# Performance work log

Measured on AMD Instinct MI355X. Metric: run time of the kernel, lower is better.

The kernel has to match this reference:

```python
import jax, jax.numpy as jnp
import numpy as np

B = 512      # molecules
F = 256      # FPSize
PH = 512     # ProjectHeadSize
H = 256      # TransformerHiddenSize
FFN = 1024   # TransformerFFNSize
NH = 8       # TransformerNumHeads
L = 2        # TransformerEncoderLayers
MAXP = 24    # max singlebond_num
EPS_BN = 1e-6
EPS_LN = 1e-5

def _make_ragged():
    sbn = (np.arange(B) % MAXP) + 1            # deterministic ragged sizes, all >= 1
    pair_mol = np.repeat(np.arange(B), sbn)
    pair_pos = np.concatenate([np.arange(n) for n in sbn])
    return sbn, pair_mol, pair_pos

def setup_inputs():
    sbn, pm, pp = _make_ragged()
    P = int(sbn.sum())  # 6336 fragment pairs
    keys = iter(jax.random.split(jax.random.key(0), 64))
    def lin(fi, fo):
        return (jax.random.normal(next(keys), (fi, fo), jnp.float32) / np.sqrt(fi),
                jnp.zeros((fo,), jnp.float32))
    d = {}
    d['mol_emb'] = jax.random.normal(next(keys), (B, F), jnp.float32)
    d['frag_emb_raw'] = jax.random.normal(next(keys), (2 * P, F), jnp.float32)
    for p in ('mol', 'frag', 'view'):
        d[p + '_W1'], d[p + '_b1'] = lin(F, PH)
        d[p + '_g'] = jnp.ones((PH,), jnp.float32)
        d[p + '_be'] = jnp.zeros((PH,), jnp.float32)
        d[p + '_W2'], d[p + '_b2'] = lin(PH, PH // 2)
    d['enc_in_W'], d['enc_in_b'] = lin(F, H)
    d['enc_out_W'], d['enc_out_b'] = lin(H, F)
    def stk(fi, fo):
        return (jax.random.normal(next(keys), (L, fi, fo), jnp.float32) / np.sqrt(fi),
                jnp.zeros((L, fo), jnp.float32))
    d['Wq'], d['bq'] = stk(H, H)
    d['Wk'], d['bk'] = stk(H, H)
    d['Wv'], d['bv'] = stk(H, H)
    d['Wo'], d['bo'] = stk(H, H)
    d['Wf1'], d['bf1'] = stk(H, FFN)
    d['Wf2'], d['bf2'] = stk(FFN, H)
    d['ln1_g'] = jnp.ones((L, H), jnp.float32); d['ln1_b'] = jnp.zeros((L, H), jnp.float32)
    d['ln2_g'] = jnp.ones((L, H), jnp.float32); d['ln2_b'] = jnp.zeros((L, H), jnp.float32)
    d['singlebond_num'] = jnp.asarray(sbn, jnp.int32)
    d['pair_mol_idx'] = jnp.asarray(pm, jnp.int32)
    d['pair_pos_idx'] = jnp.asarray(pp, jnp.int32)
    return d

def _ln(x, g, b):
    mu = x.mean(-1, keepdims=True)
    v = ((x - mu) ** 2).mean(-1, keepdims=True)
    return (x - mu) * jax.lax.rsqrt(v + EPS_LN) * g + b

def _proj_head(x, W1, b1, g, be, W2, b2):
    # Linear -> BatchNorm1d (train-mode batch stats, eps=1e-6) -> ReLU -> Linear (dropout=identity in eval)
    h = x @ W1 + b1
    mu = h.mean(0)
    v = h.var(0)
    h = jax.nn.relu((h - mu) * jax.lax.rsqrt(v + EPS_BN) * g + be)
    return h @ W2 + b2

def _l2norm(x):
    return x / jnp.maximum(jnp.linalg.norm(x, axis=1, keepdims=True), 1e-12)

def _attn(x, Wq, bq, Wk, bk, Wv, bv, Wo, bo):
    b, s, _ = x.shape
    dh = H // NH
    q = (x @ Wq + bq).reshape(b, s, NH, dh)
    k = (x @ Wk + bk).reshape(b, s, NH, dh)
    v = (x @ Wv + bv).reshape(b, s, NH, dh)
    a = jax.nn.softmax(jnp.einsum('bqhd,bkhd->bhqk', q, k) / np.sqrt(dh), axis=-1)
    return jnp.einsum('bhqk,bkhd->bqhd', a, v).reshape(b, s, H) @ Wo + bo

def reference(mol_emb, frag_emb_raw,
              mol_W1, mol_b1, mol_g, mol_be, mol_W2, mol_b2,
              frag_W1, frag_b1, frag_g, frag_be, frag_W2, frag_b2,
              view_W1, view_b1, view_g, view_be, view_W2, view_b2,
              enc_in_W, enc_in_b, enc_out_W, enc_out_b,
              ln1_g, ln1_b, Wq, bq, Wk, bk, Wv, bv, Wo, bo,
              ln2_g, ln2_b, Wf1, bf1, Wf2, bf2,
              singlebond_num, pair_mol_idx, pair_pos_idx):
    mol_proj = _l2norm(_proj_head(mol_emb, mol_W1, mol_b1, mol_g, mol_be, mol_W2, mol_b2))
    # sum the two complementary fragment embeddings per single bond: view(P,2,F).sum(1)
    P = frag_emb_raw.shape[0] // 2
    pairs = frag_emb_raw.reshape(P, 2, F).sum(axis=1)  # [P, F]
    frag_proj = _l2norm(_proj_head(pairs, frag_W1, frag_b1, frag_g, frag_be, frag_W2, frag_b2))
    sim = frag_proj @ frag_proj.T  # [P, P] pairwise dot-sim
    # ragged pack into [B, MAXP, F] (zero padding, no attention mask, as in original)
    batched = jnp.zeros((B, MAXP, F), pairs.dtype).at[pair_mol_idx, pair_pos_idx].set(pairs)
    h = batched @ enc_in_W + enc_in_b
    for l in range(L):  # pre-LN encoder layers (Graphormer-style EncoderLayer)
        h = h + _attn(_ln(h, ln1_g[l], ln1_b[l]), Wq[l], bq[l], Wk[l], bk[l], Wv[l], bv[l], Wo[l], bo[l])
        y = _ln(h, ln2_g[l], ln2_b[l])
        h = h + (jax.nn.gelu(y @ Wf1[l] + bf1[l]) @ Wf2[l] + bf2[l])
    enc = h @ enc_out_W + enc_out_b  # [B, MAXP, F]
    counts = jnp.maximum(singlebond_num, 1)
    mask = (jnp.arange(MAXP)[None, :] < counts[:, None]).astype(enc.dtype)
    readout = (enc * mask[:, :, None]).sum(axis=1) / counts[:, None].astype(enc.dtype)
    view_proj = _l2norm(_proj_head(readout, view_W1, view_b1, view_g, view_be, view_W2, view_b2))
    return (mol_proj, view_proj, sim)
```

## Files before the change

kernel.cpp:

```cpp
#include <hip/hip_runtime.h>
#include <hip/hip_bf16.h>

#define B_    512
#define F_    256
#define PH_   512
#define PH2_  256
#define H_    256
#define FFN_  1024
#define NH_   8
#define DH_   32
#define L_    2
#define MAXP_ 24
#define T_    (B_*MAXP_)
#define P_    6336
#define NFLT  5878016

typedef __hip_bfloat16 bf16;
typedef __attribute__((ext_vector_type(8))) short short8;
typedef __attribute__((ext_vector_type(4))) float floatx4;
typedef __attribute__((ext_vector_type(4))) ushort ushortx4;

__device__ float  g_arena[5*1024*1024];
__device__ float  g_small[1<<20];
__device__ float  g_par[6*1024*1024];
__device__ ushort g_parb[6*1024*1024];
__device__ ushort g_bf[41*1024*1024];
__device__ int    g_flag[4];

__device__ __forceinline__ float  u2f(ushort u){ return __uint_as_float(((unsigned)u)<<16); }
__device__ __forceinline__ ushort f2u(float f){ return __bfloat16_as_ushort(__float2bfloat16(f)); }

__device__ __forceinline__ void gll16(const ushort* g, ushort* l){
  __builtin_amdgcn_global_load_lds((const __attribute__((address_space(1))) void*)g,
                                   (__attribute__((address_space(3))) void*)l, 16, 0, 0);
}

__device__ const int d_coff[41] = {
  0,131072,3375104,3506176,3506688,3507200,3507712,3638784,3639040,3770112,
  3770624,3771136,3771648,3902720,3902976,4034048,4034560,4035072,4035584,4166656,
  4166912,4232448,4232704,4298240,4298496,4429568,4430080,4561152,4561664,4692736,
  4693248,4824320,4824832,5349120,5351168,5875456,5875968,5876480,5876992,5877504,
  5878016};

__device__ const int t_src[20] = {3375104,3507712,3639040,3771648,3902976,4035584,4166912,4232704,
  4298496,4430080,4561664,4364032,4495616,4627200,4693248,4758784,4824832,5086976,5351168,5613312};
__device__ const int t_dst[20] = {0,131072,262144,393216,524288,655360,786432,851968,
  917504,983040,1048576,1114112,1179648,1245184,1310720,1376256,1441792,1703936,1966080,2228224};
__device__ const int t_K[20] = {256,512,256,512,256,512,256,256,256,256,256,256,256,256,256,256,256,256,1024,1024};
__device__ const int t_N[20] = {512,256,512,256,512,256,256,256,256,256,256,256,256,256,256,256,1024,1024,256,256};
__device__ const int t_tp[21] = {0,32,64,96,128,160,192,208,224,240,256,272,288,304,320,336,352,416,480,544,608};

struct Ptrs { const void* p[40]; };

__global__ __launch_bounds__(256) void FraSICL_42322607735332_kernel(const unsigned* __restrict__ molg,
                                                                     float* __restrict__ batched0,
                                                                     float* __restrict__ stats){
  int i = blockIdx.x*256 + threadIdx.x;
  if (i == 0) g_flag[0] = (molg[0] == 0x3F803F80u) ? 1 : 0;
  if (i < 3*1024) stats[i] = 0.f;
  if (i < T_*H_/2) batched0[i] = 0.f;
}

__global__ __launch_bounds__(256) void k_cast_all(Ptrs ps, float* __restrict__ of, ushort* __restrict__ ob){
  int i = (blockIdx.x*256 + threadIdx.x) * 4;
  if (i >= NFLT) return;
  int lo = 0, hi = 40;
  while (lo + 1 < hi){ int mid = (lo+hi)>>1; if (i >= d_coff[mid]) lo = mid; else hi = mid; }
  int local = i - d_coff[lo];
  float4 v;
  if (g_flag[0]){
    ushortx4 u = *(const ushortx4*)((const ushort*)ps.p[lo] + local);
    v.x = u2f(u[0]); v.y = u2f(u[1]); v.z = u2f(u[2]); v.w = u2f(u[3]);
  } else {
    v = *(const float4*)((const float*)ps.p[lo] + local);
  }
  *(float4*)(of + i) = v;
  ushortx4 o; o[0]=f2u(v.x); o[1]=f2u(v.y); o[2]=f2u(v.z); o[3]=f2u(v.w);
  *(ushortx4*)(ob + i) = o;
}

__global__ __launch_bounds__(256) void k_wtT(const ushort* __restrict__ src, ushort* __restrict__ dst,
                                             const float* __restrict__ par, float* __restrict__ bqkv){
  __shared__ ushort tile[64*65];
  int b = blockIdx.x;
  if (b >= 608){
    int i = (b - 608)*256 + threadIdx.x;
    if (i < 2*768){
      int l = i / 768, n = i % 768;
      const float* s = (n < 256) ? par + 4429568 + l*256 + n
                     : (n < 512) ? par + 4561152 + l*256 + (n-256)
                                 : par + 4692736 + l*256 + (n-512);
      bqkv[i] = *s;
    }
    return;
  }
  int lo = 0, hi = 20;
  while (lo + 1 < hi){ int mid = (lo+hi)>>1; if (b >= t_tp[mid]) lo = mid; else hi = mid; }
  int lt = b - t_tp[lo];
  int K = t_K[lo], N = t_N[lo];
  int tn = N >> 6;
  int k0 = (lt / tn) << 6, n0 = (lt % tn) << 6;
  const ushort* sseg = src + t_src[lo];
  ushort* dseg = dst + t_dst[lo];
  int t = threadIdx.x;
  #pragma unroll
  for (int j = 0; j < 16; j++){
    int idx = t + j*256;
    int r = idx >> 6, c = idx & 63;
    tile[r*65 + c] = sseg[(size_t)(k0 + r)*N + n0 + c];
  }
  __syncthreads();
  #pragma unroll
  for (int j = 0; j < 16; j++){
    int idx = t + j*256;
    int on = idx >> 6, ok = idx & 63;
    dseg[(size_t)(n0 + on)*K + k0 + ok] = tile[ok*65 + on];
  }
}

__global__ void k_pairs_scatter(const float* __restrict__ frag, const int* __restrict__ pm,
                                const int* __restrict__ pp, ushort* __restrict__ pairs,
                                ushort* __restrict__ batched){
  int p = blockIdx.x, f = threadIdx.x;
  float v = frag[(size_t)(2*p)*F_ + f] + frag[(size_t)(2*p+1)*F_ + f];
  ushort u = f2u(v);
  pairs[(size_t)p*F_ + f] = u;
  batched[(size_t)(pm[p]*MAXP_ + pp[p])*H_ + f] = u;
}

__global__ __launch_bounds__(256) void k_mfma(const ushort* __restrict__ A, const ushort* __restrict__ Bm,
                                              const float* __restrict__ bias, void* __restrict__ Cv,
                                              size_t coff, int M, int N, int K, int act, int mode, int sym,
                                              float* __restrict__ stats)
{
  __shared__ ushort smem[17408];
  ushort* As_ = smem;
  ushort* Bs_ = smem + 4096;
  int tid = threadIdx.x;
  int wave = tid >> 6, lane = tid & 63;
  int wrow = (wave >> 1) * 64, wcol = (wave & 1) * 64;
  int quad = lane >> 4, l16 = lane & 15;
  int m0 = blockIdx.y * 128, n0 = blockIdx.x * 128;
  if (sym && m0 > n0) return;

  int srow = (wave << 5) + (lane >> 2);
  int scol = (lane & 3) << 3;
  int lbase = (wave << 5) * 32;

  floatx4 acc[4][4];
  #pragma unroll
  for (int i = 0; i < 4; i++)
    #pragma unroll
    for (int j = 0; j < 4; j++) acc[i][j] = (floatx4){0.f,0.f,0.f,0.f};

  for (int k0 = 0; k0 < K; k0 += 32){
    {
      int r0 = m0 + srow;      if (r0 > M-1) r0 = M-1;
      int r1 = m0 + srow + 16; if (r1 > M-1) r1 = M-1;
      gll16(A + (size_t)r0*K + k0 + scol, As_ + lbase);
      gll16(A + (size_t)r1*K + k0 + scol, As_ + lbase + 512);
      int q0 = n0 + srow;      if (q0 > N-1) q0 = N-1;
      int q1 = n0 + srow + 16; if (q1 > N-1) q1 = N-1;
      gll16(Bm + (size_t)q0*K + k0 + scol, Bs_ + lbase);
      gll16(Bm + (size_t)q1*K + k0 + scol, Bs_ + lbase + 512);
    }
    __syncthreads();
    short8 af[4], bfr[4];
    #pragma unroll
    for (int mi = 0; mi < 4; mi++) af[mi]  = *(short8*)&As_[(wrow + mi*16 + l16)*32 + quad*8];
    #pragma unroll
    for (int nj = 0; nj < 4; nj++) bfr[nj] = *(short8*)&Bs_[(wcol + nj*16 + l16)*32 + quad*8];
    #pragma unroll
    for (int mi = 0; mi < 4; mi++)
      #pragma unroll
      for (int nj = 0; nj < 4; nj++)
        acc[mi][nj] = __builtin_amdgcn_mfma_f32_16x16x32_bf16(af[mi], bfr[nj], acc[mi][nj], 0, 0, 0);
    __syncthreads();
  }

  int isbf = g_flag[0];
  bool bfpath = (mode == 2) || (mode == 3 && isbf);
  if (!bfpath){
    #pragma unroll
    for (int nj = 0; nj < 4; nj++){
      int col = n0 + wcol + nj*16 + l16;
      float ss = 0.f, ss2 = 0.f;
      #pragma unroll
      for (int mi = 0; mi < 4; mi++){
        #pragma unroll
        for (int r = 0; r < 4; r++){
          int row = m0 + wrow + mi*16 + quad*4 + r;
          if (row < M && col < N){
            float v = acc[mi][nj][r];
            if (bias) v += bias[col];
            if (act == 1) v = fmaxf(v, 0.f);
            else if (act == 2){
              float t = v + 0.044715f*v*v*v;
              v = 0.5f*v*(1.f + tanhf(0.7978845608028654f*t));
            }
            size_t idx = coff + (size_t)row*N + col;
            if (mode == 1) ((float*)Cv)[idx] += v; else ((float*)Cv)[idx] = v;
            if (sym && m0 != n0) ((float*)Cv)[coff + (size_t)col*N + row] = v;
            ss += v; ss2 += v*v;
          }
        }
      }
      if (stats && col < N){
        atomicAdd(&stats[col], ss);
        atomicAdd(&stats[N + col], ss2);
      }
    }
  } else {
    __syncthreads();
    ushort* Cs = smem;
    #pragma unroll
    for (int mi = 0; mi < 4; mi++)
      #pragma unroll
      for (int nj = 0; nj < 4; nj++){
        int lc = wcol + nj*16 + l16;
        int col = n0 + lc;
        #pragma unroll
        for (int r = 0; r < 4; r++){
          int lr = wrow + mi*16 + quad*4 + r;
          float v = acc[mi][nj][r];
          if (bias && col < N) v += bias[col];
          if (act == 1) v = fmaxf(v, 0.f);
          else if (act == 2){
            float t = v + 0.044715f*v*v*v;
            v = 0.5f*v*(1.f + tanhf(0.7978845608028654f*t));
          }
          Cs[lr*136 + lc] = f2u(v);
        }
      }
    __syncthreads();
    ushort* outp = (ushort*)Cv + coff;
    #pragma unroll
    for (int p = 0; p < 8; p++){
      int lr  = p*16 + (tid >> 4);
      int lcs = (tid & 15) * 8;
      int grow = m0 + lr, gcol = n0 + lcs;
      if (grow < M && gcol < N){
        if (gcol + 8 <= N)
          *(uint4*)(outp + (size_t)grow*N + gcol) = *(uint4*)&Cs[lr*136 + lcs];
        else
          for (int u = 0; u < N - gcol; u++) outp[(size_t)grow*N + gcol + u] = Cs[lr*136 + lcs + u];
      }
    }
    if (sym && m0 != n0){
      #pragma unroll
      for (int p = 0; p < 8; p++){
        int lr  = p*16 + (tid >> 4);
        int lcs = (tid & 15) * 8;
        int grow = n0 + lr, gcol = m0 + lcs;
        if (grow < N && gcol < M){
          ushort t8[8];
          #pragma unroll
          for (int u = 0; u < 8; u++) t8[u] = Cs[(lcs + u)*136 + lr];
          if (gcol + 8 <= M)
            *(uint4*)(outp + (size_t)grow*N + gcol) = *(uint4*)t8;
          else
            for (int u = 0; u < M - gcol; u++) outp[(size_t)grow*N + gcol + u] = t8[u];
        }
      }
    }
  }
}

#define SXf 260
#define SQe 776
#define SAe 264

template<int EPI>
__device__ __forceinline__ void enc_gemm(
    float* __restrict__ xr, ushort* __restrict__ qkvs, ushort* __restrict__ a2,
    const ushort* __restrict__ A_lds, const ushort* __restrict__ Bg, int ldb,
    const float* __restrict__ bias, int qc0, int wave, int lane)
{
  int l16 = lane & 15, quad = lane >> 4;
  floatx4 acc[2][4];
  #pragma unroll
  for (int i = 0; i < 2; i++)
    #pragma unroll
    for (int j = 0; j < 4; j++) acc[i][j] = (floatx4){0.f,0.f,0.f,0.f};

  const ushort* bp[4];
  #pragma unroll
  for (int nj = 0; nj < 4; nj++)
    bp[nj] = Bg + (size_t)(wave*64 + nj*16 + l16)*ldb + quad*8;

  #pragma unroll
  for (int kk = 0; kk < 8; kk++){
    short8 af[2], bfr[4];
    #pragma unroll
    for (int nj = 0; nj < 4; nj++) bfr[nj] = *(const short8*)(bp[nj] + kk*32);
    #pragma unroll
    for (int mi = 0; mi < 2; mi++) af[mi] = *(short8*)&A_lds[(mi*16 + l16)*SAe + kk*32 + quad*8];
    #pragma unroll
    for (int mi = 0; mi < 2; mi++)
      #pragma unroll
      for (int nj = 0; nj < 4; nj++)
        acc[mi][nj] = __builtin_amdgcn_mfma_f32_16x16x32_bf16(af[mi], bfr[nj], acc[mi][nj], 0, 0, 0);
  }

  #pragma unroll
  for (int mi = 0; mi < 2; mi++)
    #pragma unroll
    for (int nj = 0; nj < 4; nj++){
      int col = wave*64 + nj*16 + l16;
      #pragma unroll
      for (int r = 0; r < 4; r++){
        int row = mi*16 + quad*4 + r;
        float v = acc[mi][nj][r];
        if (EPI == 0){ if (row < 24) xr[row*SXf + col] = v + bias[col]; }
        else if (EPI == 1){ if (row < 24) qkvs[row*SQe + qc0 + col] = f2u(v + bias[col]); }
        else if (EPI == 2){ if (row < 24) xr[row*SXf + col] += bias ? (v + bias[col]) : v; }
        else {
          float t = v + bias[col];
          float u = t + 0.044715f*t*t*t;
          t = 0.5f*t*(1.f + tanhf(0.7978845608028654f*u));
          a2[row*SAe + col] = f2u(t);
        }
      }
    }
  __syncthreads();
}

__device__ __forceinline__ void enc_ln(const float* __restrict__ xr, ushort* __restrict__ abf,
    const float* __restrict__ g, const float* __restrict__ bv, int wave, int lane)
{
  for (int rr = wave; rr < 24; rr += 4){
    float4 v = *(const float4*)&xr[rr*SXf + lane*4];
    float s1 = v.x+v.y+v.z+v.w;
    float s2 = v.x*v.x+v.y*v.y+v.z*v.z+v.w*v.w;
    #pragma unroll
    for (int o = 32; o > 0; o >>= 1){ s1 += __shfl_down(s1, o, 64); s2 += __shfl_down(s2, o, 64); }
    s1 = __shfl(s1, 0, 64); s2 = __shfl(s2, 0, 64);
    float mu = s1 * (1.f/256.f);
    float rI = rsqrtf(s2 * (1.f/256.f) - mu*mu + 1e-5f);
    float4 gg = *(const float4*)(g + lane*4);
    float4 bb = *(const float4*)(bv + lane*4);
    ushortx4 o4;
    o4[0] = f2u((v.x-mu)*rI*gg.x + bb.x);
    o4[1] = f2u((v.y-mu)*rI*gg.y + bb.y);
    o4[2] = f2u((v.z-mu)*rI*gg.z + bb.z);
    o4[3] = f2u((v.w-mu)*rI*gg.w + bb.w);
    *(ushortx4*)&abf[rr*SAe + lane*4] = o4;
  }
  __syncthreads();
}

__device__ __forceinline__ void enc_attn(const ushort* __restrict__ qkvs, ushort* __restrict__ abf,
                                         int wave, int lane)
{
  int role = (lane < 24) ? 0 : ((lane >= 32 && lane < 56) ? 1 : -1);
  if (role >= 0){
    int r = lane - role*32;
    int h = wave*2 + role;
    int qb = h*32;
    float q[32];
    #pragma unroll
    for (int d8 = 0; d8 < 4; d8++){
      short8 qv = *(const short8*)&qkvs[r*SQe + qb + d8*8];
      #pragma unroll
      for (int u = 0; u < 8; u++) q[d8*8+u] = u2f((ushort)qv[u]);
    }
    float s[24]; float mx = -1e30f;
    #pragma unroll
    for (int j = 0; j < 24; j++){
      float a = 0.f;
      #pragma unroll
      for (int d8 = 0; d8 < 4; d8++){
        short8 kv = *(const short8*)&qkvs[j*SQe + 256 + qb + d8*8];
        #pragma unroll
        for (int u = 0; u < 8; u++) a += q[d8*8+u]*u2f((ushort)kv[u]);
      }
      s[j] = a * 0.17677669529663687f;
      mx = fmaxf(mx, s[j]);
    }
    float sum = 0.f;
    #pragma unroll
    for (int j = 0; j < 24; j++){ s[j] = __expf(s[j]-mx); sum += s[j]; }
    float inv = 1.f/sum;
    float o[32];
    #pragma unroll
    for (int d = 0; d < 32; d++) o[d] = 0.f;
    #pragma unroll
    for (int j = 0; j < 24; j++){
      #pragma unroll
      for (int d8 = 0; d8 < 4; d8++){
        short8 vv = *(const short8*)&qkvs[j*SQe + 512 + qb + d8*8];
        #pragma unroll
        for (int u = 0; u < 8; u++) o[d8*8+u] += s[j]*u2f((ushort)vv[u]);
      }
    }
    #pragma unroll
    for (int d8 = 0; d8 < 4; d8++){
      short8 ov;
      #pragma unroll
      for (int u = 0; u < 8; u++) ov[u] = (short)f2u(o[d8*8+u]*inv);
      *(short8*)&abf[r*SAe + qb + d8*8] = ov;
    }
  }
  __syncthreads();
}

__global__ __launch_bounds__(256, 2) void k_encoder(
    const ushort* __restrict__ batched, const int* __restrict__ sbn,
    const ushort* __restrict__ encinT, const float* __restrict__ enc_in_b,
    const ushort* __restrict__ qkvT, const float* __restrict__ bqkv,
    const ushort* __restrict__ WoT, const float* __restrict__ bo,
    const ushort* __restrict__ Wf1T, const float* __restrict__ bf1,
    const ushort* __restrict__ Wf2T, const float* __restrict__ bf2,
    const float* __restrict__ ln1g, const float* __restrict__ ln1b,
    const float* __restrict__ ln2g, const float* __restrict__ ln2b,
    const ushort* __restrict__ encoutT, const float* __restrict__ enc_out_b,
    ushort* __restrict__ ro)
{
  __shared__ float  xr[24*SXf];
  __shared__ ushort qkvs[24*SQe];
  __shared__ ushort abf[32*SAe];

  int b = blockIdx.x;
  int tid = threadIdx.x;
  int wave = tid >> 6, lane = tid & 63;
  ushort* a2 = qkvs;

  {
    short8 z = {0,0,0,0,0,0,0,0};
    for (int i = tid; i < 32*SAe/8; i += 256) *(short8*)&abf[i*8] = z;
  }
  {
    const ushort* Ag = batched + (size_t)b*24*256;
    #pragma unroll
    for (int i = 0; i < 3; i++){
      int e = (i*256 + tid)*8;
      short8 v = *(const short8*)(Ag + e);
      int row = e >> 8, col = e & 255;
      *(short8*)&abf[row*SAe + col] = v;
    }
  }
  __syncthreads();

  enc_gemm<0>(xr, qkvs, a2, abf, encinT, 256, enc_in_b, 0, wave, lane);

  #pragma unroll 1
  for (int l = 0; l < 2; l++){
    enc_ln(xr, abf, ln1g + l*256, ln1b + l*256, wave, lane);
    #pragma unroll 1
    for (int c = 0; c < 3; c++)
      enc_gemm<1>(xr, qkvs, a2, abf, qkvT + l*196608 + c*65536, 256,
                  bqkv + l*768 + c*256, c*256, wave, lane);
    enc_attn(qkvs, abf, wave, lane);
    enc_gemm<2>(xr, qkvs, a2, abf, WoT + l*65536, 256, bo + l*256, 0, wave, lane);
    enc_ln(xr, abf, ln2g + l*256, ln2b + l*256, wave, lane);
    #pragma unroll 1
    for (int c = 0; c < 4; c++){
      enc_gemm<3>(xr, qkvs, a2, abf, Wf1T + l*262144 + c*65536, 256,
                  bf1 + l*1024 + c*256, 0, wave, lane);
      enc_gemm<2>(xr, qkvs, a2, a2, Wf2T + l*262144 + c*256, 1024,
                  (c == 0) ? (bf2 + l*256) : (const float*)nullptr, 0, wave, lane);
    }
  }

  int cnum = sbn[b]; if (cnum < 1) cnum = 1;
  float* rd = (float*)abf;
  if (tid < 256){
    float s = 0.f;
    for (int p = 0; p < cnum; p++) s += xr[p*SXf + tid];
    rd[tid] = s / (float)cnum;
  }
  __syncthreads();
  {
    float a = enc_out_b[tid];
    const ushort* wr = encoutT + (size_t)tid*256;
    #pragma unroll
    for (int s8 = 0; s8 < 32; s8++){
      short8 wv = *(const short8*)(wr + s8*8);
      #pragma unroll
      for (int u = 0; u < 8; u++) a += rd[s8*8+u]*u2f((ushort)wv[u]);
    }
    ro[(size_t)b*256 + tid] = f2u(a);
  }
}

__global__ void k_bn_apply_bf(const float* __restrict__ h, const float* __restrict__ stats,
                              const float* __restrict__ g, const float* __restrict__ be,
                              ushort* __restrict__ ob, int N, float invM){
  int col = blockIdx.y*256 + threadIdx.x;
  float mu  = stats[col] * invM;
  float var = stats[N + col] * invM - mu*mu;
  float inv = rsqrtf(var + 1e-6f);
  size_t i = (size_t)blockIdx.x*N + col;
  float v = (h[i] - mu) * inv * g[col] + be[col];
  ob[i] = f2u(fmaxf(v, 0.f));
}

__global__ __launch_bounds__(256) void k_l2n_out(const float* __restrict__ x, void* __restrict__ outv,
                                                 size_t elem_off){
  int row = blockIdx.x, t = threadIdx.x;
  float v = x[(size_t)row*256 + t];
  float s = v*v;
  #pragma unroll
  for (int o = 32; o > 0; o >>= 1) s += __shfl_down(s, o, 64);
  __shared__ float red[4];
  int wave = t >> 6, lane = t & 63;
  if (lane == 0) red[wave] = s;
  __syncthreads();
  if (t == 0) red[0] = red[0]+red[1]+red[2]+red[3];
  __syncthreads();
  float sc = 1.f / fmaxf(sqrtf(red[0]), 1e-12f);
  float o = v * sc;
  size_t idx = elem_off + (size_t)row*256 + t;
  if (g_flag[0]) ((bf16*)outv)[idx] = __float2bfloat16(o);
  else           ((float*)outv)[idx] = o;
}

__global__ __launch_bounds__(256) void k_l2n_bfout(const float* __restrict__ x, ushort* __restrict__ ob){
  int wave = threadIdx.x >> 6, lane = threadIdx.x & 63;
  size_t row = (size_t)blockIdx.x*4 + wave;
  const float4 v = *(const float4*)(x + row*256 + lane*4);
  float s = v.x*v.x+v.y*v.y+v.z*v.z+v.w*v.w;
  #pragma unroll
  for (int o = 32; o > 0; o >>= 1) s += __shfl_down(s, o, 64);
  s = __shfl(s, 0, 64);
  float sc = 1.f / fmaxf(sqrtf(s), 1e-12f);
  ushortx4 o4;
  o4[0] = f2u(v.x*sc); o4[1] = f2u(v.y*sc); o4[2] = f2u(v.z*sc); o4[3] = f2u(v.w*sc);
  *(ushortx4*)(ob + row*256 + lane*4) = o4;
}


extern "C" void kernel_launch(void* const* d_in, const int* in_sizes, int n_in,
                              void* d_out, int out_size, void* d_ws, size_t ws_size,
                              hipStream_t stream) {
  (void)in_sizes; (void)n_in; (void)d_ws; (void)ws_size; (void)out_size;

  void *p_arena=nullptr,*p_small=nullptr,*p_par=nullptr,*p_parb=nullptr,*p_bf=nullptr;
  hipGetSymbolAddress(&p_arena, HIP_SYMBOL(g_arena));
  hipGetSymbolAddress(&p_small, HIP_SYMBOL(g_small));
  hipGetSymbolAddress(&p_par,   HIP_SYMBOL(g_par));
  hipGetSymbolAddress(&p_parb,  HIP_SYMBOL(g_parb));
  hipGetSymbolAddress(&p_bf,    HIP_SYMBOL(g_bf));
  float*  arena = (float*)p_arena;
  float*  small = (float*)p_small;
  float*  par   = (float*)p_par;
  ushort* parb  = (ushort*)p_parb;
  ushort* bfb   = (ushort*)p_bf;

  const float *mol_b1=par+3506176, *mol_g=par+3506688, *mol_be=par+3507200, *mol_b2=par+3638784;
  const float *frag_b1=par+3770112, *frag_g=par+3770624, *frag_be=par+3771136, *frag_b2=par+3902720;
  const float *view_b1=par+4034048, *view_g=par+4034560, *view_be=par+4035072, *view_b2=par+4166656;
  const float *enc_in_b=par+4232448, *enc_out_b=par+4298240;
  const float *bo=par+4824320, *bf1=par+5349120, *bf2=par+5875456;
  const float *ln1_g=par+5875968, *ln1_b=par+5876480, *ln2_g=par+5876992, *ln2_b=par+5877504;
  const ushort *molemb_b = parb + 0;
  const float  *frag_f   = par  + 131072;
  const int* sbn = (const int*)d_in[40];
  const int* pm  = (const int*)d_in[41];
  const int* pp  = (const int*)d_in[42];

  ushort* WT = bfb + 38469632;
  const ushort *molW1T=WT+0, *molW2T=WT+131072, *fragW1T=WT+262144, *fragW2T=WT+393216;
  const ushort *viewW1T=WT+524288, *viewW2T=WT+655360, *encinT=WT+786432, *encoutT=WT+851968;
  const ushort *qkvT=WT+917504, *WoT=WT+1310720, *Wf1T=WT+1441792, *Wf2T=WT+1966080;

  const size_t TH = (size_t)T_*H_;
  ushort* pairs_bf    = bfb;
  ushort* fragh1_bf   = bfb + 1622016;
  ushort* fragproj_bf = bfb + 4866048;
  ushort* batched_bf  = bfb + 6488064;
  ushort* ro_bf       = bfb + 38076416;
  ushort* h1b_bf      = bfb + 38207488;
  float* fragh1_f = arena;
  float* fragproj = arena + 3244032;
  float* tmp  = small;
  float* h1b  = small + 131072;
  float* stats= small + 393216;
  float* statsMol  = stats;
  float* statsFrag = stats + 1024;
  float* statsView = stats + 2048;
  float* bqkvf = small + 427008;

  const size_t OFF_MOL  = 0;
  const size_t OFF_VIEW = (size_t)B_*PH2_;
  const size_t OFF_SIM  = 2*(size_t)B_*PH2_;

  FraSICL_42322607735332_kernel<<<(int)(TH/2+255)/256, 256, 0, stream>>>(
      (const unsigned*)d_in[4], (float*)batched_bf, stats);
  Ptrs ps;
  for (int i = 0; i < 40; i++) ps.p[i] = d_in[i];
  k_cast_all<<<(NFLT/4+255)/256, 256, 0, stream>>>(ps, par, parb);
  k_wtT<<<614, 256, 0, stream>>>(parb, bfb + 38469632, par, bqkvf);

  k_mfma<<<dim3(PH_/128, B_/128), 256, 0, stream>>>(molemb_b, molW1T, mol_b1, h1b, 0, B_, PH_, F_, 0, 0, 0, statsMol);
  k_bn_apply_bf<<<dim3(B_, PH_/256), 256, 0, stream>>>(h1b, statsMol, mol_g, mol_be, h1b_bf, PH_, 1.f/B_);
  k_mfma<<<dim3(PH2_/128, B_/128), 256, 0, stream>>>(h1b_bf, molW2T, mol_b2, tmp, 0, B_, PH2_, PH_, 0, 0, 0, nullptr);
  k_l2n_out<<<B_, 256, 0, stream>>>(tmp, d_out, OFF_MOL);

  k_pairs_scatter<<<P_, 256, 0, stream>>>(frag_f, pm, pp, pairs_bf, batched_bf);
  k_mfma<<<dim3(PH_/128, (P_+127)/128), 256, 0, stream>>>(pairs_bf, fragW1T, frag_b1, fragh1_f, 0, P_, PH_, F_, 0, 0, 0, statsFrag);
  k_bn_apply_bf<<<dim3(P_, PH_/256), 256, 0, stream>>>(fragh1_f, statsFrag, frag_g, frag_be, fragh1_bf, PH_, 1.f/P_);
  k_mfma<<<dim3(PH2_/128, (P_+127)/128), 256, 0, stream>>>(fragh1_bf, fragW2T, frag_b2, fragproj, 0, P_, PH2_, PH_, 0, 0, 0, nullptr);
  k_l2n_bfout<<<P_/4, 256, 0, stream>>>(fragproj, fragproj_bf);
  k_mfma<<<dim3((P_+127)/128, (P_+127)/128), 256, 0, stream>>>(fragproj_bf, fragproj_bf, nullptr, d_out, OFF_SIM, P_, P_, PH2_, 0, 3, 1, nullptr);

  k_encoder<<<B_, 256, 0, stream>>>(batched_bf, sbn,
      encinT, enc_in_b, qkvT, bqkvf, WoT, bo, Wf1T, bf1, Wf2T, bf2,
      ln1_g, ln1_b, ln2_g, ln2_b, encoutT, enc_out_b, ro_bf);

  k_mfma<<<dim3(PH_/128, B_/128), 256, 0, stream>>>(ro_bf, viewW1T, view_b1, h1b, 0, B_, PH_, F_, 0, 0, 0, statsView);
  k_bn_apply_bf<<<dim3(B_, PH_/256), 256, 0, stream>>>(h1b, statsView, view_g, view_be, h1b_bf, PH_, 1.f/B_);
  k_mfma<<<dim3(PH2_/128, B_/128), 256, 0, stream>>>(h1b_bf, viewW2T, view_b2, tmp, 0, B_, PH2_, PH_, 0, 0, 0, nullptr);
  k_l2n_out<<<B_, 256, 0, stream>>>(tmp, d_out, OFF_VIEW);
}
```

Baseline: 821.7 us.

## Pack encoder weights into MFMA fragment order and use cheaper GELU tanh

Adds a k_wpack kernel that rearranges the encoder weights (enc_in, QKV, Wo, FFN1, FFN2) into 16x32 tiles laid out in MFMA fragment order, so each lane in enc_gemm loads its B fragment from one contiguous 16-byte chunk instead of strided rows. The GELU epilogue computes tanh through __expf, and the enc_out projection now reads the original row-major weights with a strided per-column access. The unused act==2 path is removed from k_mfma. This costs one extra small packing launch per call, and the GELU result differs slightly numerically.

```diff
diff --git a/kernel.cpp b/kernel.cpp
--- a/kernel.cpp
+++ b/kernel.cpp
@@ -50,6 +50,14 @@
 __device__ const int t_N[20] = {512,256,512,256,512,256,256,256,256,256,256,256,256,256,256,256,1024,1024,256,256};
 __device__ const int t_tp[21] = {0,32,64,96,128,160,192,208,224,240,256,272,288,304,320,336,352,416,480,544,608};
 
+__device__ const int w_src[13] = {4166912,4298496,4430080,4561664,4364032,4495616,4627200,
+  4693248,4758784,4824832,5086976,5351168,5613312};
+__device__ const int w_dst[13] = {0,65536,131072,196608,262144,327680,393216,
+  458752,524288,589824,851968,1114112,1376256};
+__device__ const int w_K[13] = {256,256,256,256,256,256,256,256,256,256,256,1024,1024};
+__device__ const int w_N[13] = {256,256,256,256,256,256,256,256,256,1024,1024,256,256};
+__device__ const int w_tp[14] = {0,16,32,48,64,80,96,112,128,144,208,272,336,400};
+
 struct Ptrs { const void* p[40]; };
 
 __global__ __launch_bounds__(256) void FraSICL_42322607735332_kernel(const unsigned* __restrict__ molg,
@@ -115,6 +123,39 @@
     int idx = t + j*256;
     int on = idx >> 6, ok = idx & 63;
     dseg[(size_t)(n0 + on)*K + k0 + ok] = tile[ok*65 + on];
+  }
+}
+
+__global__ __launch_bounds__(256) void k_wpack(const ushort* __restrict__ src, ushort* __restrict__ dst){
+  __shared__ ushort tile[64*65];
+  int b = blockIdx.x;
+  int lo = 0, hi = 13;
+  while (lo + 1 < hi){ int mid = (lo+hi)>>1; if (b >= w_tp[mid]) lo = mid; else hi = mid; }
+  int lt = b - w_tp[lo];
+  int K = w_K[lo], N = w_N[lo];
+  int nn = N >> 6;
+  int k0 = (lt / nn) << 6, n0 = (lt % nn) << 6;
+  const ushort* s = src + w_src[lo];
+  int t = threadIdx.x;
+  #pragma unroll
+  for (int j = 0; j < 16; j++){
+    int idx = t + j*256;
+    int r = idx >> 6, c = idx & 63;
+    tile[r*65 + c] = s[(size_t)(k0 + r)*N + n0 + c];
+  }
+  __syncthreads();
+  int KT = K >> 5;
+  ushort* d = dst + w_dst[lo];
+  #pragma unroll
+  for (int i = 0; i < 8; i++){
+    int ntl = i >> 1, ktl = i & 1;
+    size_t base = ((size_t)((n0 >> 4) + ntl) * KT + (k0 >> 5) + ktl) * 512;
+    #pragma unroll
+    for (int j = 0; j < 2; j++){
+      int off = t + j*256;
+      int quad = off >> 7, l16 = (off >> 3) & 15, e = off & 7;
+      d[base + off] = tile[(ktl*32 + quad*8 + e)*65 + ntl*16 + l16];
+    }
   }
 }
 
@@ -194,10 +235,6 @@
             float v = acc[mi][nj][r];
             if (bias) v += bias[col];
             if (act == 1) v = fmaxf(v, 0.f);
-            else if (act == 2){
-              float t = v + 0.044715f*v*v*v;
-              v = 0.5f*v*(1.f + tanhf(0.7978845608028654f*t));
-            }
             size_t idx = coff + (size_t)row*N + col;
             if (mode == 1) ((float*)Cv)[idx] += v; else ((float*)Cv)[idx] = v;
             if (sym && m0 != n0) ((float*)Cv)[coff + (size_t)col*N + row] = v;
@@ -225,10 +262,6 @@
           float v = acc[mi][nj][r];
           if (bias && col < N) v += bias[col];
           if (act == 1) v = fmaxf(v, 0.f);
-          else if (act == 2){
-            float t = v + 0.044715f*v*v*v;
-            v = 0.5f*v*(1.f + tanhf(0.7978845608028654f*t));
-          }
           Cs[lr*136 + lc] = f2u(v);
         }
       }
@@ -273,7 +306,7 @@
 template<int EPI>
 __device__ __forceinline__ void enc_gemm(
     float* __restrict__ xr, ushort* __restrict__ qkvs, ushort* __restrict__ a2,
-    const ushort* __restrict__ A_lds, const ushort* __restrict__ Bg, int ldb,
+    const ushort* __restrict__ A_lds, const ushort* __restrict__ pk, int KT, int nt0, int kt0,
     const float* __restrict__ bias, int qc0, int wave, int lane)
 {
   int l16 = lane & 15, quad = lane >> 4;
@@ -286,13 +319,13 @@
   const ushort* bp[4];
   #pragma unroll
   for (int nj = 0; nj < 4; nj++)
-    bp[nj] = Bg + (size_t)(wave*64 + nj*16 + l16)*ldb + quad*8;
+    bp[nj] = pk + ((size_t)(nt0 + wave*4 + nj)*KT + kt0)*512 + lane*8;
 
   #pragma unroll
   for (int kk = 0; kk < 8; kk++){
     short8 af[2], bfr[4];
     #pragma unroll
-    for (int nj = 0; nj < 4; nj++) bfr[nj] = *(const short8*)(bp[nj] + kk*32);
+    for (int nj = 0; nj < 4; nj++) bfr[nj] = *(const short8*)(bp[nj] + kk*512);
     #pragma unroll
     for (int mi = 0; mi < 2; mi++) af[mi] = *(short8*)&A_lds[(mi*16 + l16)*SAe + kk*32 + quad*8];
     #pragma unroll
@@ -315,10 +348,11 @@
         else if (EPI == 1){ if (row < 24) qkvs[row*SQe + qc0 + col] = f2u(v + bias[col]); }
         else if (EPI == 2){ if (row < 24) xr[row*SXf + col] += bias ? (v + bias[col]) : v; }
         else {
-          float t = v + bias[col];
-          float u = t + 0.044715f*t*t*t;
-          t = 0.5f*t*(1.f + tanhf(0.7978845608028654f*u));
-          a2[row*SAe + col] = f2u(t);
+          float t0 = v + bias[col];
+          float u = 0.7978845608028654f*(t0 + 0.044715f*t0*t0*t0);
+          float e = __expf(2.f*u);
+          float th = 1.f - 2.f/(e + 1.f);
+          a2[row*SAe + col] = f2u(0.5f*t0*(1.f + th));
         }
       }
     }
@@ -406,14 +440,14 @@
 
 __global__ __launch_bounds__(256, 2) void k_encoder(
     const ushort* __restrict__ batched, const int* __restrict__ sbn,
-    const ushort* __restrict__ encinT, const float* __restrict__ enc_in_b,
-    const ushort* __restrict__ qkvT, const float* __restrict__ bqkv,
-    const ushort* __restrict__ WoT, const float* __restrict__ bo,
-    const ushort* __restrict__ Wf1T, const float* __restrict__ bf1,
-    const ushort* __restrict__ Wf2T, const float* __restrict__ bf2,
+    const ushort* __restrict__ encinP, const float* __restrict__ enc_in_b,
+    const ushort* __restrict__ qkvP, const float* __restrict__ bqkv,
+    const ushort* __restrict__ WoP, const float* __restrict__ bo,
+    const ushort* __restrict__ Wf1P, const float* __restrict__ bf1,
+    const ushort* __restrict__ Wf2P, const float* __restrict__ bf2,
     const float* __restrict__ ln1g, const float* __restrict__ ln1b,
     const float* __restrict__ ln2g, const float* __restrict__ ln2b,
-    const ushort* __restrict__ encoutT, const float* __restrict__ enc_out_b,
+    const ushort* __restrict__ encoutO, const float* __restrict__ enc_out_b,
     ushort* __restrict__ ro)
 {
   __shared__ float  xr[24*SXf];
@@ -441,23 +475,23 @@
   }
   __syncthreads();
 
-  enc_gemm<0>(xr, qkvs, a2, abf, encinT, 256, enc_in_b, 0, wave, lane);
+  enc_gemm<0>(xr, qkvs, a2, abf, encinP, 8, 0, 0, enc_in_b, 0, wave, lane);
 
   #pragma unroll 1
   for (int l = 0; l < 2; l++){
     enc_ln(xr, abf, ln1g + l*256, ln1b + l*256, wave, lane);
     #pragma unroll 1
     for (int c = 0; c < 3; c++)
-      enc_gemm<1>(xr, qkvs, a2, abf, qkvT + l*196608 + c*65536, 256,
+      enc_gemm<1>(xr, qkvs, a2, abf, qkvP + l*196608 + c*65536, 8, 0, 0,
                   bqkv + l*768 + c*256, c*256, wave, lane);
     enc_attn(qkvs, abf, wave, lane);
-    enc_gemm<2>(xr, qkvs, a2, abf, WoT + l*65536, 256, bo + l*256, 0, wave, lane);
+    enc_gemm<2>(xr, qkvs, a2, abf, WoP + l*65536, 8, 0, 0, bo + l*256, 0, wave, lane);
     enc_ln(xr, abf, ln2g + l*256, ln2b + l*256, wave, lane);
     #pragma unroll 1
     for (int c = 0; c < 4; c++){
-      enc_gemm<3>(xr, qkvs, a2, abf, Wf1T + l*262144 + c*65536, 256,
+      enc_gemm<3>(xr, qkvs, a2, abf, Wf1P + l*262144, 8, c*16, 0,
                   bf1 + l*1024 + c*256, 0, wave, lane);
-      enc_gemm<2>(xr, qkvs, a2, a2, Wf2T + l*262144 + c*256, 1024,
+      enc_gemm<2>(xr, qkvs, a2, a2, Wf2P + l*262144, 32, 0, c*8,
                   (c == 0) ? (bf2 + l*256) : (const float*)nullptr, 0, wave, lane);
     }
   }
@@ -472,13 +506,9 @@
   __syncthreads();
   {
     float a = enc_out_b[tid];
-    const ushort* wr = encoutT + (size_t)tid*256;
-    #pragma unroll
-    for (int s8 = 0; s8 < 32; s8++){
-      short8 wv = *(const short8*)(wr + s8*8);
-      #pragma unroll
-      for (int u = 0; u < 8; u++) a += rd[s8*8+u]*u2f((ushort)wv[u]);
-    }
+    const ushort* wc = encoutO + tid;
+    #pragma unroll 8
+    for (int k = 0; k < 256; k++) a += rd[k]*u2f(wc[(size_t)k*256]);
     ro[(size_t)b*256 + tid] = f2u(a);
   }
 }
@@ -561,8 +591,14 @@
 
   ushort* WT = bfb + 38469632;
   const ushort *molW1T=WT+0, *molW2T=WT+131072, *fragW1T=WT+262144, *fragW2T=WT+393216;
-  const ushort *viewW1T=WT+524288, *viewW2T=WT+655360, *encinT=WT+786432, *encoutT=WT+851968;
-  const ushort *qkvT=WT+917504, *WoT=WT+1310720, *Wf1T=WT+1441792, *Wf2T=WT+1966080;
+  const ushort *viewW1T=WT+524288, *viewW2T=WT+655360;
+  ushort* PK = bfb + 40960000;
+  const ushort *encinP = PK + 0;
+  const ushort *qkvP   = PK + 65536;
+  const ushort *WoP    = PK + 458752;
+  const ushort *Wf1P   = PK + 589824;
+  const ushort *Wf2P   = PK + 1114112;
+  const ushort *encoutO= parb + 4232704;
 
   const size_t TH = (size_t)T_*H_;
   ushort* pairs_bf    = bfb;
@@ -591,6 +627,7 @@
   for (int i = 0; i < 40; i++) ps.p[i] = d_in[i];
   k_cast_all<<<(NFLT/4+255)/256, 256, 0, stream>>>(ps, par, parb);
   k_wtT<<<614, 256, 0, stream>>>(parb, bfb + 38469632, par, bqkvf);
+  k_wpack<<<400, 256, 0, stream>>>(parb, PK);
 
   k_mfma<<<dim3(PH_/128, B_/128), 256, 0, stream>>>(molemb_b, molW1T, mol_b1, h1b, 0, B_, PH_, F_, 0, 0, 0, statsMol);
   k_bn_apply_bf<<<dim3(B_, PH_/256), 256, 0, stream>>>(h1b, statsMol, mol_g, mol_be, h1b_bf, PH_, 1.f/B_);
@@ -605,8 +642,8 @@
   k_mfma<<<dim3((P_+127)/128, (P_+127)/128), 256, 0, stream>>>(fragproj_bf, fragproj_bf, nullptr, d_out, OFF_SIM, P_, P_, PH2_, 0, 3, 1, nullptr);
 
   k_encoder<<<B_, 256, 0, stream>>>(batched_bf, sbn,
-      encinT, enc_in_b, qkvT, bqkvf, WoT, bo, Wf1T, bf1, Wf2T, bf2,
-      ln1_g, ln1_b, ln2_g, ln2_b, encoutT, enc_out_b, ro_bf);
+      encinP, enc_in_b, qkvP, bqkvf, WoP, bo, Wf1P, bf1, Wf2P, bf2,
+      ln1_g, ln1_b, ln2_g, ln2_b, encoutO, enc_out_b, ro_bf);
 
   k_mfma<<<dim3(PH_/128, B_/128), 256, 0, stream>>>(ro_bf, viewW1T, view_b1, h1b, 0, B_, PH_, F_, 0, 0, 0, statsView);
   k_bn_apply_bf<<<dim3(B_, PH_/256), 256, 0, stream>>>(h1b, statsView, view_g, view_be, h1b_bf, PH_, 1.f/B_);
```

Result: faster. 702.4 us (-14.5%).
